# Performance work log

Measured on AMD Instinct MI355X. Metric: run time of the kernel, lower is better.

## Reference

```python
import jax, jax.numpy as jnp
import numpy as np

# Model hyper-parameters (from CMRET __init__ defaults)
N_A, F, H, K, NK, L = 4096, 128, 4, 15, 50, 6
CUTOFF, TEMP, BOX, N_Z = 5.0, 2.0, 40.0, 100
DH = F // H  # per-head dim


def setup_inputs() -> dict:
    key = jax.random.key(0)
    ks = jax.random.split(key, 12)
    Z = jax.random.randint(ks[0], (1, N_A), 0, N_Z)
    R = jax.random.uniform(ks[1], (1, N_A, 3), dtype=jnp.float32) * BOX
    batch = jnp.ones((1, N_A, 1), jnp.float32)
    g = lambda k, shp, s: jax.random.normal(k, shp, jnp.float32) * s
    emb = g(ks[2], (N_Z, F), 1.0)
    Wq = g(ks[3], (L, F, F), F ** -0.5)
    Wk = g(ks[4], (L, F, F), F ** -0.5)
    Wv = g(ks[5], (L, F, 3 * F), F ** -0.5)
    We_k = g(ks[6], (L, NK, F), NK ** -0.5)
    be_k = jnp.zeros((L, F), jnp.float32)
    We_v = g(ks[7], (L, NK, 3 * F), NK ** -0.5)
    be_v = jnp.zeros((L, 3 * F), jnp.float32)
    ln_g = jnp.ones((F,), jnp.float32)
    ln_b = jnp.zeros((F,), jnp.float32)
    Wo1 = g(ks[8], (F, F), F ** -0.5)
    Wo2 = g(ks[9], (F, 1), F ** -0.5)
    return dict(Z=Z, R=R, batch=batch, emb=emb, Wq=Wq, Wk=Wk, Wv=Wv,
                We_k=We_k, be_k=be_k, We_v=We_v, be_v=be_v,
                ln_g=ln_g, ln_b=ln_b, Wo1=Wo1, Wo2=Wo2)


def reference(Z, R, batch, emb, Wq, Wk, Wv, We_k, be_k, We_v, be_v, ln_g, ln_b, Wo1, Wo2):
    n_a = Z.shape[1]
    r = R[0]                                  # (n_a, 3)
    b = batch[..., 0]                         # (1, n_a)
    bm = (b.T @ b) == 0                       # (n_a, n_a) cross-molecule mask
    # --- Distance: k-nearest-neighbour selection (gather-based) ---
    sq = jnp.sum(r * r, -1)
    d2 = sq[:, None] + sq[None, :] - 2.0 * (r @ r.T)
    d2 = jnp.where(bm | jnp.eye(n_a, dtype=bool), 1e9, jnp.maximum(d2, 0.0))
    _, idxs = jax.lax.top_k(-d2, K)           # (n_a, K) neighbour indices
    vec = r[idxs] - r[:, None, :]             # (n_a, K, 3)
    d = jnp.sqrt(jnp.sum(vec * vec, -1) + 1e-12)
    vec_norm = vec / d[..., None]
    # --- Gaussian RBF * cosine cutoff edge features ---
    mu = jnp.linspace(0.0, CUTOFF, NK, dtype=jnp.float32)
    delta = CUTOFF / NK
    cut = 0.5 * (jnp.cos(jnp.pi * d / CUTOFF) + 1.0) * (d <= CUTOFF)
    e = jnp.exp(-((d[..., None] - mu) ** 2) / (2.0 * delta * delta)) * cut[..., None]
    # --- embedding and channel init ---
    s = emb[Z[0]]                             # (n_a, F) scalar channel
    o = jnp.zeros_like(s)                     # residual accumulator
    v = jnp.zeros((n_a, 3, F), s.dtype)       # vector channel
    scale = jnp.asarray(1.0 / np.sqrt(DH * TEMP), jnp.float32)
    # --- attention interaction stack ---
    for l in range(L):
        q = (s @ Wq[l]).reshape(n_a, H, DH)
        kk = s @ Wk[l]
        val = s @ Wv[l]                       # (n_a, 3F)
        ek = jax.nn.silu(e @ We_k[l] + be_k[l])   # (n_a, K, F) edge key filter
        ev = jax.nn.silu(e @ We_v[l] + be_v[l])   # (n_a, K, 3F) edge value filter
        kh = (kk[idxs] * ek).reshape(n_a, K, H, DH)
        logits = jnp.einsum('nhd,nkhd->nkh', q, kh) * scale
        attn = jax.nn.softmax(logits, axis=1) * cut[..., None]
        wf = jnp.repeat(attn, DH, axis=-1)        # (n_a, K, F) per-channel weights
        m1, m2, m3 = jnp.split(val[idxs] * ev, 3, axis=-1)
        ds = jnp.sum(wf * m1, axis=1)             # scalar message (n_a, F)
        dv = jnp.sum((wf * m2)[:, :, None, :] * vec_norm[..., None]
                     + (wf * m3)[:, :, None, :] * v[idxs], axis=1)
        s = s + ds
        o = o + ds
        v = v + dv
    # --- final LayerNorm + readout ---
    mean = o.mean(-1, keepdims=True)
    var = o.var(-1, keepdims=True)
    o = (o - mean) / jnp.sqrt(var + 1e-5) * ln_g + ln_b
    h = jax.nn.silu(o @ Wo1) @ Wo2            # (n_a, 1) per-atom contribution
    return jnp.sum(h * batch[0], axis=0, keepdims=True)  # (1, 1) energy
```

## Files before the change

### kernel.cpp

```cpp
#include <hip/hip_runtime.h>
#include <math.h>

#define NATOMS  4096
#define FDIM    128
#define NHEAD   4
#define DHEAD   32
#define KNBR    15
#define NKER    50
#define NLAYER  6
#define QKVW    640
#define LISTCAP 768

typedef __attribute__((ext_vector_type(8))) short short8;
typedef __attribute__((ext_vector_type(4))) float f32x4;

__device__ __forceinline__ float silu_f(float x) { return x / (1.0f + __expf(-x)); }

__device__ __forceinline__ unsigned long long shfl_xor_u64(unsigned long long v, int m) {
    unsigned lo = (unsigned)v, hi = (unsigned)(v >> 32);
    lo = (unsigned)__shfl_xor((int)lo, m);
    hi = (unsigned)__shfl_xor((int)hi, m);
    return ((unsigned long long)hi << 32) | lo;
}
__device__ __forceinline__ unsigned long long min_u64(unsigned long long a, unsigned long long b) {
    return a < b ? a : b;
}
__device__ __forceinline__ int spread3(int v) {
    return (v & 1) | ((v & 2) << 2) | ((v & 4) << 4) | ((v & 8) << 6);
}

__global__ __launch_bounds__(1024) void morton_kernel(
    const float* __restrict__ R, const float* __restrict__ batch,
    int* __restrict__ perm, float* __restrict__ Rs,
    float* __restrict__ batch_s, int* __restrict__ cell_start)
{
    __shared__ int hist[4096];
    __shared__ int tscan[1024];
    const int t = threadIdx.x;
    int codes[4];
    float xs[4], ys[4], zs[4];
    #pragma unroll
    for (int u = 0; u < 4; ++u) hist[t*4 + u] = 0;
    __syncthreads();
    #pragma unroll
    for (int u = 0; u < 4; ++u) {
        int i = t + u*1024;
        float x = R[i*3+0], y = R[i*3+1], z = R[i*3+2];
        xs[u] = x; ys[u] = y; zs[u] = z;
        int cx = min(15, max(0, (int)(x * 0.4f)));
        int cy = min(15, max(0, (int)(y * 0.4f)));
        int cz = min(15, max(0, (int)(z * 0.4f)));
        int code = spread3(cx) | (spread3(cy) << 1) | (spread3(cz) << 2);
        codes[u] = code;
        atomicAdd(&hist[code], 1);
    }
    __syncthreads();
    int loc[4], s0 = 0;
    #pragma unroll
    for (int u = 0; u < 4; ++u) { loc[u] = hist[t*4 + u]; s0 += loc[u]; }
    tscan[t] = s0;
    __syncthreads();
    for (int off = 1; off < 1024; off <<= 1) {
        int v = tscan[t];
        int a = (t >= off) ? tscan[t - off] : 0;
        __syncthreads();
        tscan[t] = v + a;
        __syncthreads();
    }
    int run = tscan[t] - s0;
    #pragma unroll
    for (int u = 0; u < 4; ++u) {
        hist[t*4 + u] = run;
        cell_start[t*4 + u] = run;
        run += loc[u];
    }
    if (t == 0) cell_start[4096] = NATOMS;
    __syncthreads();
    #pragma unroll
    for (int u = 0; u < 4; ++u) {
        int i = t + u*1024;
        int r = atomicAdd(&hist[codes[u]], 1);
        perm[r] = i;
        Rs[r*3+0] = xs[u]; Rs[r*3+1] = ys[u]; Rs[r*3+2] = zs[u];
        batch_s[r] = batch[i];
    }
}

__global__ __launch_bounds__(64) void knn_kernel(
    const float* __restrict__ Rs, const float* __restrict__ batch_s,
    const int* __restrict__ cell_start,
    int* __restrict__ idxs, float* __restrict__ cutw,
    float* __restrict__ vecn, unsigned short* __restrict__ eA)
{
    __shared__ unsigned long long list[LISTCAP];
    __shared__ int   ridx[LISTCAP];
    __shared__ float e_lds[16][68];
    __shared__ float dist[KNBR];
    __shared__ float cutl[KNBR];
    __shared__ int   selr[KNBR];
    __shared__ int   cnt;
    const int r = blockIdx.x, t = threadIdx.x;
    if (t == 0) cnt = 0;
    for (int x = t; x < 16*68; x += 64) ((float*)e_lds)[x] = 0.0f;
    const float xi = Rs[r*3+0], yi = Rs[r*3+1], zi = Rs[r*3+2];
    const float bi = batch_s[r];
    const float sqi = xi*xi + yi*yi + zi*zi;
    const int cx = min(15, max(0, (int)(xi * 0.4f)));
    const int cy = min(15, max(0, (int)(yi * 0.4f)));
    const int cz = min(15, max(0, (int)(zi * 0.4f)));
    __syncthreads();

    for (int cid = t; cid < 343; cid += 64) {
        int nx = cx + (cid % 7) - 3;
        int ny = cy + ((cid / 7) % 7) - 3;
        int nz = cz + (cid / 49) - 3;
        if (nx < 0 || nx > 15 || ny < 0 || ny > 15 || nz < 0 || nz > 15) continue;
        int code = spread3(nx) | (spread3(ny) << 1) | (spread3(nz) << 2);
        int s0 = cell_start[code], s1 = cell_start[code + 1];
        for (int r2 = s0; r2 < s1; ++r2) {
            if (r2 == r) continue;
            float xj = Rs[r2*3+0], yj = Rs[r2*3+1], zj = Rs[r2*3+2];
            if (bi * batch_s[r2] == 0.0f) continue;
            float sqj = xj*xj + yj*yj + zj*zj;
            float d2 = sqi + sqj - 2.0f*(xi*xj + yi*yj + zi*zj);
            d2 = fmaxf(d2, 0.0f);
            int slot = atomicAdd(&cnt, 1);
            if (slot < LISTCAP) {
                list[slot] = ((unsigned long long)__float_as_uint(d2) << 32) | (unsigned)slot;
                ridx[slot] = r2;
            }
        }
    }
    __syncthreads();
    const int n = min(cnt, LISTCAP);

    unsigned long long cand = ~0ull;
    for (int idx = t; idx < n; idx += 64) cand = min_u64(cand, list[idx]);
    for (int k = 0; k < KNBR; ++k) {
        unsigned long long w = cand;
        #pragma unroll
        for (int off = 1; off < 64; off <<= 1)
            w = min_u64(w, shfl_xor_u64(w, off));
        int slot = (int)(unsigned)w;
        if (t == 0) selr[k] = ridx[slot];
        if ((slot & 63) == t) {
            list[slot] = ~0ull;
            cand = ~0ull;
            for (int idx = t; idx < n; idx += 64) cand = min_u64(cand, list[idx]);
        }
        __syncthreads();
    }

    if (t < KNBR) {
        int r2 = selr[t];
        idxs[r*KNBR + t] = r2;
        float vx = Rs[r2*3+0]-xi, vy = Rs[r2*3+1]-yi, vz = Rs[r2*3+2]-zi;
        float d = sqrtf(vx*vx + vy*vy + vz*vz + 1e-12f);
        float inv = 1.0f/d;
        vecn[(r*KNBR+t)*3+0] = vx*inv;
        vecn[(r*KNBR+t)*3+1] = vy*inv;
        vecn[(r*KNBR+t)*3+2] = vz*inv;
        const float PI = 3.14159265358979323846f;
        float cutv = (d <= 5.0f) ? 0.5f*(cosf(PI*d*0.2f) + 1.0f) : 0.0f;
        cutw[r*KNBR + t] = cutv;
        dist[t] = d; cutl[t] = cutv;
    }
    __syncthreads();

    for (int x = t; x < KNBR*NKER; x += 64) {
        int k = x / NKER, jj = x % NKER;
        float d = dist[k];
        float mu = 5.0f * (float)jj / 49.0f;
        float dd = d - mu;
        e_lds[k][jj] = __expf(-dd*dd*50.0f) * cutl[k];
    }
    __syncthreads();

    const int lx = t & 15, quad = t >> 4;
    #pragma unroll
    for (int grp = 0; grp < 4; ++grp) {
        const int ks = grp >> 1, part = grp & 1;
        short8 vv;
        #pragma unroll
        for (int j = 0; j < 8; ++j) {
            float v = e_lds[lx][ks*32 + quad*8 + j];
            unsigned b = __float_as_uint(v);
            if (part == 0) vv[j] = (short)(b >> 16);
            else {
                float rr = v - __uint_as_float(b & 0xFFFF0000u);
                vv[j] = (short)(__float_as_uint(rr) >> 16);
            }
        }
        *(short8*)(eA + (size_t)r*2048 + grp*512 + t*8) = vv;
    }
}

__global__ __launch_bounds__(256) void init_kernel(
    const int* __restrict__ Z, const float* __restrict__ emb,
    const int* __restrict__ perm,
    float* __restrict__ s, float* __restrict__ o, float* __restrict__ v0)
{
    int stride = gridDim.x * blockDim.x;
    for (int idx = blockIdx.x*blockDim.x + threadIdx.x; idx < NATOMS*3*FDIM; idx += stride) {
        v0[idx] = 0.0f;
        if (idx < NATOMS*FDIM) {
            int a = idx >> 7, c = idx & 127;
            s[idx] = emb[Z[perm[a]]*FDIM + c];
            o[idx] = 0.0f;
        }
    }
}

__global__ __launch_bounds__(64) void wprep_kernel(
    const float* __restrict__ WeK, const float* __restrict__ WeV,
    unsigned short* __restrict__ Wswz)
{
    const int blk = blockIdx.x;
    const int lane = threadIdx.x;
    const int ks = blk & 1;
    const int T  = (blk >> 1) & 31;
    const int l  = blk >> 6;
    const int quad = lane >> 4, x = lane & 15;
    unsigned short* dst = Wswz + (size_t)blk*1024 + lane*8;
    for (int j = 0; j < 8; ++j) {
        int k = ks*32 + quad*8 + j;
        float w = 0.0f;
        if (k < NKER)
            w = (T < 8) ? WeK[l*NKER*FDIM + k*FDIM + T*16 + x]
                        : WeV[(size_t)l*NKER*3*FDIM + k*3*FDIM + (T-8)*16 + x];
        unsigned b = __float_as_uint(w);
        dst[j] = (unsigned short)(b >> 16);
        float r = w - __uint_as_float(b & 0xFFFF0000u);
        dst[512 + j] = (unsigned short)(__float_as_uint(r) >> 16);
    }
}

__global__ __launch_bounds__(64) void qprep_kernel(
    const float* __restrict__ Wq, const float* __restrict__ Wk,
    const float* __restrict__ Wv, unsigned short* __restrict__ Qswz)
{
    const int blk = blockIdx.x;
    const int lane = threadIdx.x;
    const int ks = blk & 3;
    const int ct = (blk >> 2) % 40;
    const int l  = blk / 160;
    const int quad = lane >> 4, lx = lane & 15;
    const int col = ct*16 + lx;
    unsigned short* dst = Qswz + (size_t)blk*1024 + lane*8;
    for (int j = 0; j < 8; ++j) {
        int k = ks*32 + quad*8 + j;
        float w;
        if (col < 128)      w = Wq[l*16384 + k*128 + col];
        else if (col < 256) w = Wk[l*16384 + k*128 + (col-128)];
        else                w = Wv[(size_t)l*49152 + k*384 + (col-256)];
        unsigned b = __float_as_uint(w);
        dst[j] = (unsigned short)(b >> 16);
        float r = w - __uint_as_float(b & 0xFFFF0000u);
        dst[512 + j] = (unsigned short)(__float_as_uint(r) >> 16);
    }
}

__global__ __launch_bounds__(128) void proj_kernel(
    const float* __restrict__ S, const unsigned short* __restrict__ Qswz,
    float* __restrict__ QKV, int l)
{
    const int rt = blockIdx.x;
    const int t = threadIdx.x, wave = t >> 6, lane = t & 63;
    const int quad = lane >> 4, lx = lane & 15;
    const int cg = blockIdx.y*2 + wave;

    short8 ah[4], al[4];
    const float* srow = S + (size_t)(rt*16 + lx)*FDIM;
    #pragma unroll
    for (int ks = 0; ks < 4; ++ks) {
        float v[8];
        *(f32x4*)&v[0] = *(const f32x4*)(srow + ks*32 + quad*8);
        *(f32x4*)&v[4] = *(const f32x4*)(srow + ks*32 + quad*8 + 4);
        #pragma unroll
        for (int j = 0; j < 8; ++j) {
            unsigned b = __float_as_uint(v[j]);
            ah[ks][j] = (short)(b >> 16);
            float r = v[j] - __uint_as_float(b & 0xFFFF0000u);
            al[ks][j] = (short)(__float_as_uint(r) >> 16);
        }
    }
    for (int ci = 0; ci < 10; ++ci) {
        const int ct = cg*10 + ci;
        const unsigned short* wp = Qswz + (size_t)((l*40 + ct)*4)*1024 + lane*8;
        f32x4 acc = {0.0f, 0.0f, 0.0f, 0.0f};
        #pragma unroll
        for (int ks = 0; ks < 4; ++ks) {
            short8 bh = *(const short8*)(wp + ks*1024);
            short8 bl = *(const short8*)(wp + ks*1024 + 512);
            acc = __builtin_amdgcn_mfma_f32_16x16x32_bf16(ah[ks], bh, acc, 0, 0, 0);
            acc = __builtin_amdgcn_mfma_f32_16x16x32_bf16(ah[ks], bl, acc, 0, 0, 0);
            acc = __builtin_amdgcn_mfma_f32_16x16x32_bf16(al[ks], bh, acc, 0, 0, 0);
        }
        const int col = ct*16 + lx;
        #pragma unroll
        for (int r = 0; r < 4; ++r)
            QKV[(size_t)(rt*16 + quad*4 + r)*QKVW + col] = acc[r];
    }
}

__global__ __launch_bounds__(1024) void attn_kernel(
    const float* __restrict__ QKV, const int* __restrict__ idxs,
    const float* __restrict__ cutw, const float* __restrict__ vecn,
    const unsigned short* __restrict__ eA, const unsigned short* __restrict__ Wswz,
    const float* __restrict__ beK, const float* __restrict__ beV,
    float* __restrict__ s, float* __restrict__ o,
    const float* __restrict__ vin, float* __restrict__ vout, int l)
{
    __shared__ __align__(16) float fbuf[2][KNBR][513];
    __shared__ int   nidx[2][KNBR];
    __shared__ float cutv[2][KNBR];
    __shared__ float vnc[2][KNBR][3];
    __shared__ float attns[2][KNBR][NHEAD];

    const int t = threadIdx.x;
    const int half = t >> 9, tl = t & 511;
    const int i = blockIdx.x*2 + half;
    const int wave = tl >> 6, lane = t & 63;
    const int quad = lane >> 4, lx = lane & 15;

    if (tl < KNBR) {
        nidx[half][tl] = idxs[i*KNBR + tl];
        cutv[half][tl] = cutw[i*KNBR + tl];
        vnc[half][tl][0] = vecn[(i*KNBR+tl)*3+0];
        vnc[half][tl][1] = vecn[(i*KNBR+tl)*3+1];
        vnc[half][tl][2] = vecn[(i*KNBR+tl)*3+2];
    }
    const unsigned short* ea = eA + (size_t)i*2048 + lane*8;
    short8 eh[2], el[2];
    eh[0] = *(const short8*)(ea + 0*512);
    el[0] = *(const short8*)(ea + 1*512);
    eh[1] = *(const short8*)(ea + 2*512);
    el[1] = *(const short8*)(ea + 3*512);
    __syncthreads();

    #pragma unroll
    for (int tt = 0; tt < 4; ++tt) {
        const int T = wave*4 + tt;
        const int col = T*16 + lx;
        f32x4 acc = {0.0f, 0.0f, 0.0f, 0.0f};
        #pragma unroll
        for (int ks = 0; ks < 2; ++ks) {
            const unsigned short* wp = Wswz + ((size_t)((l*32+T)*2+ks))*1024 + lane*8;
            short8 bh = *(const short8*)wp;
            short8 bl = *(const short8*)(wp + 512);
            acc = __builtin_amdgcn_mfma_f32_16x16x32_bf16(eh[ks], bh, acc, 0, 0, 0);
            acc = __builtin_amdgcn_mfma_f32_16x16x32_bf16(eh[ks], bl, acc, 0, 0, 0);
            acc = __builtin_amdgcn_mfma_f32_16x16x32_bf16(el[ks], bh, acc, 0, 0, 0);
        }
        const float b = (col < FDIM) ? beK[l*FDIM + col]
                                     : beV[(size_t)l*3*FDIM + (col - FDIM)];
        const int goff = (col < FDIM) ? (FDIM + col) : (2*FDIM + (col - FDIM));
        #pragma unroll
        for (int r = 0; r < 4; ++r) {
            int k = quad*4 + r;
            if (k < KNBR) {
                float f = silu_f(acc[r] + b);
                float g = QKV[(size_t)nidx[half][k]*QKVW + goff];
                fbuf[half][k][col] = f * g;
            }
        }
    }
    __syncthreads();

    float pre[KNBR];
    if (tl < FDIM) {
        const int c = tl, h = c >> 5;
        const float q = QKV[(size_t)i*QKVW + c];
        float lg[KNBR];
        #pragma unroll
        for (int k = 0; k < KNBR; ++k) {
            float p = q * fbuf[half][k][c];
            p += __shfl_xor(p, 1);
            p += __shfl_xor(p, 2);
            p += __shfl_xor(p, 4);
            p += __shfl_xor(p, 8);
            p += __shfl_xor(p, 16);
            lg[k] = p * 0.125f;
        }
        float m = -1e30f;
        #pragma unroll
        for (int k = 0; k < KNBR; ++k) m = fmaxf(m, lg[k]);
        float ssum = 0.0f;
        #pragma unroll
        for (int k = 0; k < KNBR; ++k) { lg[k] = __expf(lg[k]-m); ssum += lg[k]; }
        float inv = 1.0f/ssum;
        if ((c & 31) == 0) {
            #pragma unroll
            for (int k = 0; k < KNBR; ++k) attns[half][k][h] = lg[k]*inv*cutv[half][k];
        }
    } else if (tl < 2*FDIM) {
        const int cc = tl - FDIM;
        #pragma unroll
        for (int k = 0; k < KNBR; ++k) pre[k] = fbuf[half][k][2*FDIM + cc];
    } else {
        const int cc = (tl < 3*FDIM) ? (tl - 2*FDIM) : (tl - 3*FDIM);
        #pragma unroll
        for (int k = 0; k < KNBR; ++k) pre[k] = fbuf[half][k][3*FDIM + cc];
    }
    __syncthreads();

    float d3[3] = {0.0f, 0.0f, 0.0f};
    if (tl < FDIM) {
        const int c = tl, h = c >> 5;
        float ds = 0.0f;
        #pragma unroll
        for (int k = 0; k < KNBR; ++k) ds += attns[half][k][h]*fbuf[half][k][FDIM + c];
        s[i*FDIM + c] += ds;
        o[i*FDIM + c] += ds;
    } else if (tl < 2*FDIM) {
        const int cc = tl - FDIM, h = cc >> 5;
        float d0 = 0.0f, d1 = 0.0f, d2 = 0.0f;
        #pragma unroll
        for (int k = 0; k < KNBR; ++k) {
            float w = attns[half][k][h]*pre[k];
            d0 += w*vnc[half][k][0]; d1 += w*vnc[half][k][1]; d2 += w*vnc[half][k][2];
        }
        fbuf[half][0][2*FDIM + cc] = d0;
        fbuf[half][1][2*FDIM + cc] = d1;
        fbuf[half][2][2*FDIM + cc] = d2;
    } else if (tl < 3*FDIM) {
        const int cc = tl - 2*FDIM, h = cc >> 5;
        #pragma unroll
        for (int k = 0; k < 8; ++k) {
            float w = attns[half][k][h]*pre[k];
            const float* vb = vin + (size_t)nidx[half][k]*3*FDIM + cc;
            d3[0] += w*vb[0*FDIM]; d3[1] += w*vb[1*FDIM]; d3[2] += w*vb[2*FDIM];
        }
    } else {
        const int cc = tl - 3*FDIM, h = cc >> 5;
        float e0 = 0.0f, e1 = 0.0f, e2 = 0.0f;
        #pragma unroll
        for (int k = 8; k < KNBR; ++k) {
            float w = attns[half][k][h]*pre[k];
            const float* vb = vin + (size_t)nidx[half][k]*3*FDIM + cc;
            e0 += w*vb[0*FDIM]; e1 += w*vb[1*FDIM]; e2 += w*vb[2*FDIM];
        }
        fbuf[half][3][2*FDIM + cc] = e0;
        fbuf[half][4][2*FDIM + cc] = e1;
        fbuf[half][5][2*FDIM + cc] = e2;
    }
    __syncthreads();

    if (tl >= 2*FDIM && tl < 3*FDIM) {
        const int cc = tl - 2*FDIM;
        #pragma unroll
        for (int x = 0; x < 3; ++x) {
            size_t off = (size_t)i*3*FDIM + x*FDIM + cc;
            vout[off] = vin[off] + fbuf[half][x][2*FDIM + cc]
                                 + fbuf[half][3+x][2*FDIM + cc] + d3[x];
        }
    }
}

__global__ __launch_bounds__(128) void final_kernel(
    const float* __restrict__ o, const float* __restrict__ lng, const float* __restrict__ lnb,
    const float* __restrict__ Wo1, const float* __restrict__ Wo2,
    const float* __restrict__ batch, const int* __restrict__ perm,
    float* __restrict__ hout)
{
    __shared__ float red[128];
    __shared__ float on[128];
    const int i = blockIdx.x, t = threadIdx.x;
    float x = o[i*FDIM + t];
    red[t] = x; __syncthreads();
    for (int off = 64; off > 0; off >>= 1) { if (t < off) red[t] += red[t+off]; __syncthreads(); }
    float mean = red[0] * (1.0f/128.0f);
    __syncthreads();
    float xm = x - mean;
    red[t] = xm*xm; __syncthreads();
    for (int off = 64; off > 0; off >>= 1) { if (t < off) red[t] += red[t+off]; __syncthreads(); }
    float var = red[0] * (1.0f/128.0f);
    __syncthreads();
    on[t] = xm * rsqrtf(var + 1e-5f) * lng[t] + lnb[t];
    __syncthreads();
    float acc = 0.0f;
    #pragma unroll 8
    for (int j = 0; j < 128; ++j) acc += on[j] * Wo1[j*128 + t];
    float h = silu_f(acc) * Wo2[t];
    red[t] = h; __syncthreads();
    for (int off = 64; off > 0; off >>= 1) { if (t < off) red[t] += red[t+off]; __syncthreads(); }
    if (t == 0) hout[i] = red[0] * batch[perm[i]];
}

__global__ __launch_bounds__(1024) void reduce_kernel(
    const float* __restrict__ hout, float* __restrict__ out)
{
    __shared__ float red[1024];
    const int t = threadIdx.x;
    float a = hout[t] + hout[t+1024] + hout[t+2048] + hout[t+3072];
    red[t] = a; __syncthreads();
    for (int off = 512; off > 0; off >>= 1) {
        if (t < off) red[t] += red[t+off];
        __syncthreads();
    }
    if (t == 0) out[0] = red[0];
}

extern "C" void kernel_launch(void* const* d_in, const int* in_sizes, int n_in,
                              void* d_out, int out_size, void* d_ws, size_t ws_size,
                              hipStream_t stream)
{
    const int*   Z     = (const int*)  d_in[0];
    const float* R     = (const float*)d_in[1];
    const float* batch = (const float*)d_in[2];
    const float* emb   = (const float*)d_in[3];
    const float* Wq    = (const float*)d_in[4];
    const float* Wk    = (const float*)d_in[5];
    const float* Wv    = (const float*)d_in[6];
    const float* WeK   = (const float*)d_in[7];
    const float* beK   = (const float*)d_in[8];
    const float* WeV   = (const float*)d_in[9];
    const float* beV   = (const float*)d_in[10];
    const float* lng   = (const float*)d_in[11];
    const float* lnb   = (const float*)d_in[12];
    const float* Wo1   = (const float*)d_in[13];
    const float* Wo2   = (const float*)d_in[14];
    float* out = (float*)d_out;

    float* fws = (float*)d_ws;
    float* s    = fws; fws += NATOMS*FDIM;
    float* o    = fws; fws += NATOMS*FDIM;
    float* v0   = fws; fws += NATOMS*3*FDIM;
    float* v1   = fws; fws += NATOMS*3*FDIM;
    float* qkv  = fws; fws += NATOMS*QKVW;
    float* cutw = fws; fws += NATOMS*KNBR;
    float* vecn = fws; fws += NATOMS*KNBR*3;
    float* hout = fws; fws += NATOMS;
    float* Rs   = fws; fws += NATOMS*3;
    float* bsrt = fws; fws += NATOMS;
    int*   idxs = (int*)fws; fws += NATOMS*KNBR;
    int*   perm = (int*)fws; fws += NATOMS;
    int*   cells= (int*)fws; fws += 4097;
    fws += 3;
    unsigned short* eA   = (unsigned short*)fws;
    fws += (NATOMS*2048) / 2;
    unsigned short* Wswz = (unsigned short*)fws;
    fws += (NLAYER*32*2*1024) / 2;
    unsigned short* Qswz = (unsigned short*)fws;

    morton_kernel<<<1, 1024, 0, stream>>>(R, batch, perm, Rs, bsrt, cells);
    wprep_kernel<<<NLAYER*32*2, 64, 0, stream>>>(WeK, WeV, Wswz);
    qprep_kernel<<<NLAYER*40*4, 64, 0, stream>>>(Wq, Wk, Wv, Qswz);
    knn_kernel<<<NATOMS, 64, 0, stream>>>(Rs, bsrt, cells, idxs, cutw, vecn, eA);
    init_kernel<<<1024, 256, 0, stream>>>(Z, emb, perm, s, o, v0);
    for (int l = 0; l < NLAYER; ++l) {
        proj_kernel<<<dim3(256, 2), 128, 0, stream>>>(s, Qswz, qkv, l);
        float* vin  = (l & 1) ? v1 : v0;
        float* vout = (l & 1) ? v0 : v1;
        attn_kernel<<<NATOMS/2, 1024, 0, stream>>>(qkv, idxs, cutw, vecn, eA, Wswz,
                                                   beK, beV, s, o, vin, vout, l);
    }
    final_kernel<<<NATOMS, 128, 0, stream>>>(o, lng, lnb, Wo1, Wo2, batch, perm, hout);
    reduce_kernel<<<1, 1024, 0, stream>>>(hout, out);
}
```

Measured before the change: 519.9 us.

## Fuse key logits into edge-filter MFMA epilogue and merge weight-prep kernels

The waves computing the key-filter tiles now form q·(k*ek) partial dot products directly in registers. They reduce them with lane shuffles and write per-head logits to a small shared array, so key features are no longer stored to shared memory. Softmax moves to four threads per atom, and the shared feature buffer shrinks from 513 to 385 columns per neighbour, which may improve occupancy. The two weight-swizzle prep kernels are merged into one launch to save launch overhead.

```diff
diff --git a/kernel.cpp b/kernel.cpp
--- a/kernel.cpp
+++ b/kernel.cpp
@@ -10,6 +10,7 @@
 #define NLAYER  6
 #define QKVW    640
 #define LISTCAP 768
+#define FB      385
 
 typedef __attribute__((ext_vector_type(8))) short short8;
 typedef __attribute__((ext_vector_type(4))) float f32x4;
@@ -211,52 +212,50 @@
     }
 }
 
-__global__ __launch_bounds__(64) void wprep_kernel(
+__global__ __launch_bounds__(64) void prep_kernel(
     const float* __restrict__ WeK, const float* __restrict__ WeV,
-    unsigned short* __restrict__ Wswz)
-{
-    const int blk = blockIdx.x;
+    const float* __restrict__ Wq, const float* __restrict__ Wk,
+    const float* __restrict__ Wv,
+    unsigned short* __restrict__ Wswz, unsigned short* __restrict__ Qswz)
+{
     const int lane = threadIdx.x;
-    const int ks = blk & 1;
-    const int T  = (blk >> 1) & 31;
-    const int l  = blk >> 6;
-    const int quad = lane >> 4, x = lane & 15;
-    unsigned short* dst = Wswz + (size_t)blk*1024 + lane*8;
-    for (int j = 0; j < 8; ++j) {
-        int k = ks*32 + quad*8 + j;
-        float w = 0.0f;
-        if (k < NKER)
-            w = (T < 8) ? WeK[l*NKER*FDIM + k*FDIM + T*16 + x]
-                        : WeV[(size_t)l*NKER*3*FDIM + k*3*FDIM + (T-8)*16 + x];
-        unsigned b = __float_as_uint(w);
-        dst[j] = (unsigned short)(b >> 16);
-        float r = w - __uint_as_float(b & 0xFFFF0000u);
-        dst[512 + j] = (unsigned short)(__float_as_uint(r) >> 16);
-    }
-}
-
-__global__ __launch_bounds__(64) void qprep_kernel(
-    const float* __restrict__ Wq, const float* __restrict__ Wk,
-    const float* __restrict__ Wv, unsigned short* __restrict__ Qswz)
-{
-    const int blk = blockIdx.x;
-    const int lane = threadIdx.x;
-    const int ks = blk & 3;
-    const int ct = (blk >> 2) % 40;
-    const int l  = blk / 160;
-    const int quad = lane >> 4, lx = lane & 15;
-    const int col = ct*16 + lx;
-    unsigned short* dst = Qswz + (size_t)blk*1024 + lane*8;
-    for (int j = 0; j < 8; ++j) {
-        int k = ks*32 + quad*8 + j;
-        float w;
-        if (col < 128)      w = Wq[l*16384 + k*128 + col];
-        else if (col < 256) w = Wk[l*16384 + k*128 + (col-128)];
-        else                w = Wv[(size_t)l*49152 + k*384 + (col-256)];
-        unsigned b = __float_as_uint(w);
-        dst[j] = (unsigned short)(b >> 16);
-        float r = w - __uint_as_float(b & 0xFFFF0000u);
-        dst[512 + j] = (unsigned short)(__float_as_uint(r) >> 16);
+    if (blockIdx.x < NLAYER*32*2) {
+        const int blk = blockIdx.x;
+        const int ks = blk & 1;
+        const int T  = (blk >> 1) & 31;
+        const int l  = blk >> 6;
+        const int quad = lane >> 4, x = lane & 15;
+        unsigned short* dst = Wswz + (size_t)blk*1024 + lane*8;
+        for (int j = 0; j < 8; ++j) {
+            int k = ks*32 + quad*8 + j;
+            float w = 0.0f;
+            if (k < NKER)
+                w = (T < 8) ? WeK[l*NKER*FDIM + k*FDIM + T*16 + x]
+                            : WeV[(size_t)l*NKER*3*FDIM + k*3*FDIM + (T-8)*16 + x];
+            unsigned b = __float_as_uint(w);
+            dst[j] = (unsigned short)(b >> 16);
+            float r = w - __uint_as_float(b & 0xFFFF0000u);
+            dst[512 + j] = (unsigned short)(__float_as_uint(r) >> 16);
+        }
+    } else {
+        const int blk = blockIdx.x - NLAYER*32*2;
+        const int ks = blk & 3;
+        const int ct = (blk >> 2) % 40;
+        const int l  = blk / 160;
+        const int quad = lane >> 4, lx = lane & 15;
+        const int col = ct*16 + lx;
+        unsigned short* dst = Qswz + (size_t)blk*1024 + lane*8;
+        for (int j = 0; j < 8; ++j) {
+            int k = ks*32 + quad*8 + j;
+            float w;
+            if (col < 128)      w = Wq[l*16384 + k*128 + col];
+            else if (col < 256) w = Wk[l*16384 + k*128 + (col-128)];
+            else                w = Wv[(size_t)l*49152 + k*384 + (col-256)];
+            unsigned b = __float_as_uint(w);
+            dst[j] = (unsigned short)(b >> 16);
+            float r = w - __uint_as_float(b & 0xFFFF0000u);
+            dst[512 + j] = (unsigned short)(__float_as_uint(r) >> 16);
+        }
     }
 }
 
@@ -311,10 +310,11 @@
     float* __restrict__ s, float* __restrict__ o,
     const float* __restrict__ vin, float* __restrict__ vout, int l)
 {
-    __shared__ __align__(16) float fbuf[2][KNBR][513];
+    __shared__ __align__(16) float fbuf[2][KNBR][FB];
     __shared__ int   nidx[2][KNBR];
     __shared__ float cutv[2][KNBR];
     __shared__ float vnc[2][KNBR][3];
+    __shared__ float lgs[2][KNBR][NHEAD];
     __shared__ float attns[2][KNBR][NHEAD];
 
     const int t = threadIdx.x;
@@ -338,69 +338,107 @@
     el[1] = *(const short8*)(ea + 3*512);
     __syncthreads();
 
-    #pragma unroll
-    for (int tt = 0; tt < 4; ++tt) {
-        const int T = wave*4 + tt;
-        const int col = T*16 + lx;
-        f32x4 acc = {0.0f, 0.0f, 0.0f, 0.0f};
-        #pragma unroll
-        for (int ks = 0; ks < 2; ++ks) {
-            const unsigned short* wp = Wswz + ((size_t)((l*32+T)*2+ks))*1024 + lane*8;
-            short8 bh = *(const short8*)wp;
-            short8 bl = *(const short8*)(wp + 512);
-            acc = __builtin_amdgcn_mfma_f32_16x16x32_bf16(eh[ks], bh, acc, 0, 0, 0);
-            acc = __builtin_amdgcn_mfma_f32_16x16x32_bf16(eh[ks], bl, acc, 0, 0, 0);
-            acc = __builtin_amdgcn_mfma_f32_16x16x32_bf16(el[ks], bh, acc, 0, 0, 0);
-        }
-        const float b = (col < FDIM) ? beK[l*FDIM + col]
-                                     : beV[(size_t)l*3*FDIM + (col - FDIM)];
-        const int goff = (col < FDIM) ? (FDIM + col) : (2*FDIM + (col - FDIM));
-        #pragma unroll
-        for (int r = 0; r < 4; ++r) {
-            int k = quad*4 + r;
-            if (k < KNBR) {
-                float f = silu_f(acc[r] + b);
-                float g = QKV[(size_t)nidx[half][k]*QKVW + goff];
-                fbuf[half][k][col] = f * g;
+    if (wave < 2) {
+        float pk[4][2] = {};
+        #pragma unroll
+        for (int tt = 0; tt < 4; ++tt) {
+            const int T = wave*4 + tt;
+            const int col = T*16 + lx;
+            const int hl = tt >> 1;
+            f32x4 acc = {0.0f, 0.0f, 0.0f, 0.0f};
+            #pragma unroll
+            for (int ks = 0; ks < 2; ++ks) {
+                const unsigned short* wp = Wswz + ((size_t)((l*32+T)*2+ks))*1024 + lane*8;
+                short8 bh = *(const short8*)wp;
+                short8 bl = *(const short8*)(wp + 512);
+                acc = __builtin_amdgcn_mfma_f32_16x16x32_bf16(eh[ks], bh, acc, 0, 0, 0);
+                acc = __builtin_amdgcn_mfma_f32_16x16x32_bf16(eh[ks], bl, acc, 0, 0, 0);
+                acc = __builtin_amdgcn_mfma_f32_16x16x32_bf16(el[ks], bh, acc, 0, 0, 0);
+            }
+            const float b = beK[l*FDIM + col];
+            const float q = QKV[(size_t)i*QKVW + col];
+            #pragma unroll
+            for (int r = 0; r < 4; ++r) {
+                int k = quad*4 + r;
+                if (k < KNBR) {
+                    float f = silu_f(acc[r] + b);
+                    float g = QKV[(size_t)nidx[half][k]*QKVW + FDIM + col];
+                    pk[r][hl] += q * f * g;
+                }
+            }
+        }
+        #pragma unroll
+        for (int off = 1; off < 16; off <<= 1) {
+            #pragma unroll
+            for (int r = 0; r < 4; ++r) {
+                pk[r][0] += __shfl_xor(pk[r][0], off);
+                pk[r][1] += __shfl_xor(pk[r][1], off);
+            }
+        }
+        if (lx == 0) {
+            #pragma unroll
+            for (int r = 0; r < 4; ++r) {
+                int k = quad*4 + r;
+                if (k < KNBR) {
+                    lgs[half][k][wave*2+0] = pk[r][0] * 0.125f;
+                    lgs[half][k][wave*2+1] = pk[r][1] * 0.125f;
+                }
+            }
+        }
+    } else {
+        #pragma unroll
+        for (int tt = 0; tt < 4; ++tt) {
+            const int T = wave*4 + tt;
+            const int col = T*16 + lx;
+            f32x4 acc = {0.0f, 0.0f, 0.0f, 0.0f};
+            #pragma unroll
+            for (int ks = 0; ks < 2; ++ks) {
+                const unsigned short* wp = Wswz + ((size_t)((l*32+T)*2+ks))*1024 + lane*8;
+                short8 bh = *(const short8*)wp;
+                short8 bl = *(const short8*)(wp + 512);
+                acc = __builtin_amdgcn_mfma_f32_16x16x32_bf16(eh[ks], bh, acc, 0, 0, 0);
+                acc = __builtin_amdgcn_mfma_f32_16x16x32_bf16(eh[ks], bl, acc, 0, 0, 0);
+                acc = __builtin_amdgcn_mfma_f32_16x16x32_bf16(el[ks], bh, acc, 0, 0, 0);
+            }
+            const float b = beV[(size_t)l*3*FDIM + (col - FDIM)];
+            #pragma unroll
+            for (int r = 0; r < 4; ++r) {
+                int k = quad*4 + r;
+                if (k < KNBR) {
+                    float f = silu_f(acc[r] + b);
+                    float g = QKV[(size_t)nidx[half][k]*QKVW + FDIM + col];
+                    fbuf[half][k][col - FDIM] = f * g;
+                }
             }
         }
     }
     __syncthreads();
 
     float pre[KNBR];
+    if (tl < NHEAD) {
+        const int h = tl;
+        float m = -1e30f;
+        #pragma unroll
+        for (int k = 0; k < KNBR; ++k) m = fmaxf(m, lgs[half][k][h]);
+        float ssum = 0.0f;
+        float ex[KNBR];
+        #pragma unroll
+        for (int k = 0; k < KNBR; ++k) { ex[k] = __expf(lgs[half][k][h]-m); ssum += ex[k]; }
+        float inv = 1.0f/ssum;
+        #pragma unroll
+        for (int k = 0; k < KNBR; ++k) attns[half][k][h] = ex[k]*inv*cutv[half][k];
+    }
     if (tl < FDIM) {
-        const int c = tl, h = c >> 5;
-        const float q = QKV[(size_t)i*QKVW + c];
-        float lg[KNBR];
-        #pragma unroll
-        for (int k = 0; k < KNBR; ++k) {
-            float p = q * fbuf[half][k][c];
-            p += __shfl_xor(p, 1);
-            p += __shfl_xor(p, 2);
-            p += __shfl_xor(p, 4);
-            p += __shfl_xor(p, 8);
-            p += __shfl_xor(p, 16);
-            lg[k] = p * 0.125f;
-        }
-        float m = -1e30f;
-        #pragma unroll
-        for (int k = 0; k < KNBR; ++k) m = fmaxf(m, lg[k]);
-        float ssum = 0.0f;
-        #pragma unroll
-        for (int k = 0; k < KNBR; ++k) { lg[k] = __expf(lg[k]-m); ssum += lg[k]; }
-        float inv = 1.0f/ssum;
-        if ((c & 31) == 0) {
-            #pragma unroll
-            for (int k = 0; k < KNBR; ++k) attns[half][k][h] = lg[k]*inv*cutv[half][k];
-        }
+        #pragma unroll
+        for (int k = 0; k < KNBR; ++k) pre[k] = fbuf[half][k][tl];
     } else if (tl < 2*FDIM) {
         const int cc = tl - FDIM;
         #pragma unroll
-        for (int k = 0; k < KNBR; ++k) pre[k] = fbuf[half][k][2*FDIM + cc];
+        for (int k = 0; k < KNBR; ++k) pre[k] = fbuf[half][k][FDIM + cc];
     } else {
         const int cc = (tl < 3*FDIM) ? (tl - 2*FDIM) : (tl - 3*FDIM);
         #pragma unroll
-        for (int k = 0; k < KNBR; ++k) pre[k] = fbuf[half][k][3*FDIM + cc];
+        for (int k = 0; k < KNBR; ++k) pre[k] = fbuf[half][k][2*FDIM + cc];
     }
     __syncthreads();
 
@@ -409,7 +447,7 @@
         const int c = tl, h = c >> 5;
         float ds = 0.0f;
         #pragma unroll
-        for (int k = 0; k < KNBR; ++k) ds += attns[half][k][h]*fbuf[half][k][FDIM + c];
+        for (int k = 0; k < KNBR; ++k) ds += attns[half][k][h]*pre[k];
         s[i*FDIM + c] += ds;
         o[i*FDIM + c] += ds;
     } else if (tl < 2*FDIM) {
@@ -420,9 +458,9 @@
             float w = attns[half][k][h]*pre[k];
             d0 += w*vnc[half][k][0]; d1 += w*vnc[half][k][1]; d2 += w*vnc[half][k][2];
         }
-        fbuf[half][0][2*FDIM + cc] = d0;
-        fbuf[half][1][2*FDIM + cc] = d1;
-        fbuf[half][2][2*FDIM + cc] = d2;
+        fbuf[half][0][FDIM + cc] = d0;
+        fbuf[half][1][FDIM + cc] = d1;
+        fbuf[half][2][FDIM + cc] = d2;
     } else if (tl < 3*FDIM) {
         const int cc = tl - 2*FDIM, h = cc >> 5;
         #pragma unroll
@@ -440,9 +478,9 @@
             const float* vb = vin + (size_t)nidx[half][k]*3*FDIM + cc;
             e0 += w*vb[0*FDIM]; e1 += w*vb[1*FDIM]; e2 += w*vb[2*FDIM];
         }
-        fbuf[half][3][2*FDIM + cc] = e0;
-        fbuf[half][4][2*FDIM + cc] = e1;
-        fbuf[half][5][2*FDIM + cc] = e2;
+        fbuf[half][3][FDIM + cc] = e0;
+        fbuf[half][4][FDIM + cc] = e1;
+        fbuf[half][5][FDIM + cc] = e2;
     }
     __syncthreads();
 
@@ -451,8 +489,8 @@
         #pragma unroll
         for (int x = 0; x < 3; ++x) {
             size_t off = (size_t)i*3*FDIM + x*FDIM + cc;
-            vout[off] = vin[off] + fbuf[half][x][2*FDIM + cc]
-                                 + fbuf[half][3+x][2*FDIM + cc] + d3[x];
+            vout[off] = vin[off] + fbuf[half][x][FDIM + cc]
+                                 + fbuf[half][3+x][FDIM + cc] + d3[x];
         }
     }
 }
@@ -544,8 +582,7 @@
     unsigned short* Qswz = (unsigned short*)fws;
 
     morton_kernel<<<1, 1024, 0, stream>>>(R, batch, perm, Rs, bsrt, cells);
-    wprep_kernel<<<NLAYER*32*2, 64, 0, stream>>>(WeK, WeV, Wswz);
-    qprep_kernel<<<NLAYER*40*4, 64, 0, stream>>>(Wq, Wk, Wv, Qswz);
+    prep_kernel<<<NLAYER*32*2 + NLAYER*40*4, 64, 0, stream>>>(WeK, WeV, Wq, Wk, Wv, Wswz, Qswz);
     knn_kernel<<<NATOMS, 64, 0, stream>>>(Rs, bsrt, cells, idxs, cutw, vecn, eA);
     init_kernel<<<1024, 256, 0, stream>>>(Z, emb, perm, s, o, v0);
     for (int l = 0; l < NLAYER; ++l) {
```

Result: slower. 604.9 us (+16.3%).
